# Performance work log

Hardware: AMD Instinct MI355X
Metric: run time of the kernel (lower is better)

The kernel has to match this reference:

```python
import jax, jax.numpy as jnp
import numpy as np

# static config (matches init_kwargs)
B, H, W = 8, 64, 64
DIM, NH = 512, 16
HD = DIM // NH
WS = 8            # square window
SHIFT = 4
N = WS * WS       # tokens per window
NW = (H // WS) * (W // WS)  # windows per image
SCALE = HD ** (-0.5)
MLP_HIDDEN = int(DIM * 4.0)


def _rel_pos_index():
    coords = np.stack(np.meshgrid(np.arange(WS), np.arange(WS), indexing='ij'))  # [2,Wh,Ww]
    cf = coords.reshape(2, -1)
    rel = cf[:, :, None] - cf[:, None, :]          # [2,N,N]
    rel = rel.transpose(1, 2, 0)                    # [N,N,2]
    rel[:, :, 0] += WS - 1
    rel[:, :, 1] += WS - 1
    rel[:, :, 0] *= 2 * WS - 1
    return rel.sum(-1)                              # [N,N]

REL_IDX = jnp.asarray(_rel_pos_index())


def _attn_mask():
    img_mask = np.zeros((1, H, W, 1), np.float32)
    slices = (slice(0, -WS), slice(-WS, -SHIFT), slice(-SHIFT, None))
    cnt = 0
    for hs in slices:
        for ws in slices:
            img_mask[:, hs, ws, :] = cnt
            cnt += 1
    m = img_mask.reshape(1, H // WS, WS, W // WS, WS, 1).transpose(0, 1, 3, 2, 4, 5).reshape(-1, N)
    am = m[:, None, :] - m[:, :, None]
    return jnp.asarray(np.where(am != 0, -100.0, 0.0).astype(np.float32))  # [NW,N,N]

ATTN_MASK = _attn_mask()


def layernorm(x, g, b, eps=1e-5):
    mu = x.mean(-1, keepdims=True)
    var = ((x - mu) ** 2).mean(-1, keepdims=True)
    return (x - mu) * jax.lax.rsqrt(var + eps) * g + b


def setup_inputs() -> dict:
    key = jax.random.key(0)
    ks = jax.random.split(key, 12)
    s = 0.02
    return {
        'x': jax.random.normal(ks[0], (B, H * W, DIM), jnp.float32),
        'fundamental_context': jax.random.normal(ks[1], (B, 64), jnp.float32),
        'norm1_g': jnp.ones((DIM,), jnp.float32),
        'norm1_b': jnp.zeros((DIM,), jnp.float32),
        'qkv_w': jax.random.normal(ks[2], (DIM, 3 * DIM), jnp.float32) * s,
        'qkv_b': jnp.zeros((3 * DIM,), jnp.float32),
        'rel_bias_table': jax.random.normal(ks[3], ((2 * WS - 1) ** 2, NH), jnp.float32) * s,
        'proj_w': jax.random.normal(ks[4], (DIM, DIM), jnp.float32) * s,
        'proj_b': jnp.zeros((DIM,), jnp.float32),
        'norm2_g': jnp.ones((DIM,), jnp.float32),
        'norm2_b': jnp.zeros((DIM,), jnp.float32),
        'fc1_w': jax.random.normal(ks[5], (DIM, MLP_HIDDEN), jnp.float32) * s,
        'fc1_b': jnp.zeros((MLP_HIDDEN,), jnp.float32),
        'fc2_w': jax.random.normal(ks[6], (MLP_HIDDEN, DIM), jnp.float32) * s,
        'fc2_b': jnp.zeros((DIM,), jnp.float32),
    }


def reference(x, fundamental_context, norm1_g, norm1_b, qkv_w, qkv_b,
              rel_bias_table, proj_w, proj_b, norm2_g, norm2_b,
              fc1_w, fc1_b, fc2_w, fc2_b):
    shortcut = x
    h = layernorm(x, norm1_g, norm1_b).reshape(B, H, W, DIM)
    # cyclic shift (SW-MSA)
    h = jnp.roll(h, (-SHIFT, -SHIFT), axis=(1, 2))
    # window partition -> [B*NW, N, C]
    win = h.reshape(B, H // WS, WS, W // WS, WS, DIM).transpose(0, 1, 3, 2, 4, 5)
    win = win.reshape(B * NW, N, DIM)
    # windowed multi-head attention
    qkv = (win @ qkv_w + qkv_b).reshape(B * NW, N, 3, NH, HD).transpose(2, 0, 3, 1, 4)
    q, k, v = qkv[0] * SCALE, qkv[1], qkv[2]          # [B_,NH,N,HD]
    attn = jnp.einsum('bhnd,bhmd->bhnm', q, k)        # [B_,NH,N,N]
    bias = rel_bias_table[REL_IDX.reshape(-1)].reshape(N, N, NH).transpose(2, 0, 1)
    attn = attn + bias[None]
    attn = attn.reshape(B, NW, NH, N, N) + ATTN_MASK[None, :, None]
    attn = jax.nn.softmax(attn.reshape(B * NW, NH, N, N), axis=-1)
    out = jnp.einsum('bhnm,bhmd->bhnd', attn, v).transpose(0, 2, 1, 3).reshape(B * NW, N, DIM)
    out = out @ proj_w + proj_b
    # window reverse -> [B,H,W,C]
    out = out.reshape(B, H // WS, W // WS, WS, WS, DIM).transpose(0, 1, 3, 2, 4, 5).reshape(B, H, W, DIM)
    # reverse cyclic shift
    out = jnp.roll(out, (SHIFT, SHIFT), axis=(1, 2)).reshape(B, H * W, DIM)
    x = shortcut + out
    # MLP block
    h = layernorm(x, norm2_g, norm2_b)
    h = jax.nn.gelu(h @ fc1_w + fc1_b, approximate=False) @ fc2_w + fc2_b
    return x + h
```

## Files before the change

### kernel.cpp

```cpp
#include <hip/hip_runtime.h>
#include <cstddef>
#include <cstdint>


typedef unsigned short u16;
typedef __attribute__((ext_vector_type(8))) short short8;
typedef __attribute__((ext_vector_type(4))) float floatx4;

__device__ __forceinline__ float bf2f(u16 u) {
    union { float f; unsigned i; } w; w.i = ((unsigned)u) << 16; return w.f;
}
__device__ __forceinline__ u16 f2bf(float f) {
    union { float f; unsigned i; } w; w.f = f;
    unsigned r = w.i + 0x7FFF + ((w.i >> 16) & 1);
    return (u16)(r >> 16);
}

__device__ __forceinline__ void gload_lds16(const u16* g, u16* l) {
    __builtin_amdgcn_global_load_lds(
        (const __attribute__((address_space(1))) void*)g,
        (__attribute__((address_space(3))) void*)l, 16, 0, 0);
}

__device__ __forceinline__ float erf_fast(float x) {
    float ax = fabsf(x);
    float t = 1.0f / (1.0f + 0.3275911f * ax);
    float poly = ((((1.061405429f * t - 1.453152027f) * t + 1.421413741f) * t
                   - 0.284496736f) * t + 0.254829592f) * t;
    float er = 1.0f - poly * __expf(-ax * ax);
    return copysignf(er, x);
}

__device__ __forceinline__ int win_to_img_row(int t) {
    int win = t >> 6, n = t & 63;
    int b = win >> 6, wr = (win >> 3) & 7, wc = win & 7;
    int h = ((wr << 3) + (n >> 3) + 4) & 63;
    int w = ((wc << 3) + (n & 7) + 4) & 63;
    return (b << 12) + (h << 6) + w;
}

__global__ __launch_bounds__(256) void ln_fused(
    const float* __restrict__ x, const float* __restrict__ g,
    const float* __restrict__ b, u16* __restrict__ out, int gather)
{
    int wave = threadIdx.x >> 6, lane = threadIdx.x & 63;
    int t = blockIdx.x * 4 + wave;
    int src = gather ? win_to_img_row(t) : t;
    const float* xr = x + (size_t)src * 512 + lane * 8;
    float4 a = *(const float4*)xr;
    float4 c = *(const float4*)(xr + 4);
    float s = a.x + a.y + a.z + a.w + c.x + c.y + c.z + c.w;
    float s2 = a.x*a.x + a.y*a.y + a.z*a.z + a.w*a.w
             + c.x*c.x + c.y*c.y + c.z*c.z + c.w*c.w;
#pragma unroll
    for (int off = 32; off; off >>= 1) { s += __shfl_down(s, off); s2 += __shfl_down(s2, off); }
    s = __shfl(s, 0); s2 = __shfl(s2, 0);
    float mu = s * (1.f / 512.f);
    float var = s2 * (1.f / 512.f) - mu * mu;
    float rs = rsqrtf(var + 1e-5f);
    int col = lane * 8;
    float4 g0 = *(const float4*)(g + col), g1 = *(const float4*)(g + col + 4);
    float4 b0 = *(const float4*)(b + col), b1 = *(const float4*)(b + col + 4);
    u16 r[8];
    r[0] = f2bf((a.x - mu) * rs * g0.x + b0.x);
    r[1] = f2bf((a.y - mu) * rs * g0.y + b0.y);
    r[2] = f2bf((a.z - mu) * rs * g0.z + b0.z);
    r[3] = f2bf((a.w - mu) * rs * g0.w + b0.w);
    r[4] = f2bf((c.x - mu) * rs * g1.x + b1.x);
    r[5] = f2bf((c.y - mu) * rs * g1.y + b1.y);
    r[6] = f2bf((c.z - mu) * rs * g1.z + b1.z);
    r[7] = f2bf((c.w - mu) * rs * g1.w + b1.w);
    *(uint4*)(out + (size_t)t * 512 + col) = *(const uint4*)r;
}

__global__ __launch_bounds__(256) void transpose_all(
    const float* __restrict__ qkv_w, const float* __restrict__ proj_w,
    const float* __restrict__ fc1_w, const float* __restrict__ fc2_w,
    u16* __restrict__ qkvT, u16* __restrict__ projT,
    u16* __restrict__ fc1T, u16* __restrict__ fc2T)
{
    int bid = blockIdx.x;
    const float* W; u16* WT; int K, N, base;
    if (bid < 384)       { W = qkv_w;  WT = qkvT;  K = 512;  N = 1536; base = 0; }
    else if (bid < 512)  { W = proj_w; WT = projT; K = 512;  N = 512;  base = 384; }
    else if (bid < 1024) { W = fc1_w;  WT = fc1T;  K = 512;  N = 2048; base = 512; }
    else                 { W = fc2_w;  WT = fc2T;  K = 2048; N = 512;  base = 1024; }
    int f = (bid - base) * 256 + threadIdx.x;
    int n = f % N, kc = f / N;
    if (kc >= (K >> 3)) return;
    int k0 = kc << 3;
    u16 r[8];
#pragma unroll
    for (int j = 0; j < 8; ++j) r[j] = f2bf(W[(size_t)(k0 + j) * N + n]);
    *(uint4*)(WT + (size_t)n * K + k0) = *(const uint4*)r;
}

enum { M_QKV = 0, M_PROJ = 1, M_GELU = 2, M_FINAL = 3 };

template <int MODE, int ASRC>
__global__ __launch_bounds__(256, 4) void gemm_bt(
    const u16* __restrict__ A, int lda,
    const u16* __restrict__ BT, int ldb,
    const float* __restrict__ bias,
    void* __restrict__ outp, const float* __restrict__ auxf, int K, int ldo)
{
    __shared__ __align__(16) u16 As[128 * 64];
    __shared__ __align__(16) u16 Bs[128 * 64];

    int tid = threadIdx.x;
    int nwg = gridDim.x * gridDim.y;
    int bid = blockIdx.y * gridDim.x + blockIdx.x;
    int q8 = nwg >> 3, r8 = nwg & 7;
    int xcd = bid & 7, pos = bid >> 3;
    int swz = (xcd < r8 ? xcd * (q8 + 1)
                        : r8 * (q8 + 1) + (xcd - r8) * q8) + pos;
    int bx = swz % gridDim.x, by = swz / gridDim.x;
    int bm = by * 128, bn = bx * 128;

    int wave = tid >> 6, lane = tid & 63;
    int quad = lane >> 4, lr = lane & 15;
    int wm = (wave >> 1) * 64, wn = (wave & 1) * 64;

    floatx4 acc[4][4] = {};

    for (int k0 = 0; k0 < K; k0 += 64) {
#pragma unroll
        for (int l = 0; l < 4; ++l) {
            int f = (l << 8) + tid;
            int row = f >> 3, c = f & 7;
            int cs = c ^ (row & 7);
            int kk = k0 + (cs << 3);
            const u16* gb = BT + (size_t)(bn + row) * ldb + kk;
            gload_lds16(gb, Bs + f * 8);
            if constexpr (ASRC == 0) {
                gload_lds16(A + (size_t)(bm + row) * lda + kk, As + f * 8);
            } else {
                int m = bm + row;
                gload_lds16(A + (size_t)(((m >> 6) << 4) + (kk >> 5)) * 2048
                              + (m & 63) * 32 + (kk & 31), As + f * 8);
            }
        }
        __syncthreads();
#pragma unroll
        for (int step = 0; step < 2; ++step) {
            short8 af[4], bv[4];
            int kc = step * 4 + quad;
#pragma unroll
            for (int t = 0; t < 4; ++t) {
                int ra = wm + t * 16 + lr;
                int rb = wn + t * 16 + lr;
                af[t] = *(const short8*)(As + ra * 64 + ((kc ^ (ra & 7)) << 3));
                bv[t] = *(const short8*)(Bs + rb * 64 + ((kc ^ (rb & 7)) << 3));
            }
#pragma unroll
            for (int mt = 0; mt < 4; ++mt)
#pragma unroll
                for (int nt = 0; nt < 4; ++nt)
                    acc[mt][nt] = __builtin_amdgcn_mfma_f32_16x16x32_bf16(
                        af[mt], bv[nt], acc[mt][nt], 0, 0, 0);
        }
        __syncthreads();
    }

#pragma unroll
    for (int mt = 0; mt < 4; ++mt) {
#pragma unroll
        for (int nt = 0; nt < 4; ++nt) {
            int m0 = bm + wm + mt * 16 + quad * 4;
            int n = bn + wn + nt * 16 + lr;
#pragma unroll
            for (int i = 0; i < 4; ++i) {
                int m = m0 + i;
                float v = acc[mt][nt][i];
                if constexpr (MODE == M_QKV) {
                    v += bias[n];
                    int sel = n >> 9, head = (n >> 5) & 15, d = n & 31;
                    int wh = (m >> 6) * 16 + head, tok = m & 63;
                    ((u16*)outp)[(size_t)sel * 16777216 + (size_t)wh * 2048 + tok * 32 + d] = f2bf(v);
                } else if constexpr (MODE == M_PROJ) {
                    size_t idx = (size_t)win_to_img_row(m) * 512 + n;
                    ((float*)outp)[idx] = v + bias[n] + auxf[idx];
                } else if constexpr (MODE == M_GELU) {
                    v += bias[n];
                    float gel = 0.5f * v * (1.0f + erf_fast(v * 0.70710678118654752f));
                    ((u16*)outp)[(size_t)m * ldo + n] = f2bf(gel);
                } else {
                    size_t idx = (size_t)m * 512 + n;
                    float* o = (float*)outp;
                    float bb = bias ? bias[n] : 0.0f;
                    o[idx] = o[idx] + v + bb;
                }
            }
        }
    }
}

__global__ __launch_bounds__(256) void attn_mfma(
    const u16* __restrict__ qkv, const float* __restrict__ table,
    u16* __restrict__ outp)
{
    __shared__ __align__(8) u16 PT[4][64 * 76];
    __shared__ float blds[225];

    int w = threadIdx.x >> 6, lane = threadIdx.x & 63;
    int head = blockIdx.x & 15, win = ((blockIdx.x >> 4) << 2) + w;
    int wh = (win << 4) + head;
    int quad = lane >> 4, lr = lane & 15;
    const u16* qb = qkv + (size_t)wh * 2048;
    const u16* kb = qb + 16777216;
    const u16* vb = qb + 33554432;
    u16* PTw = PT[w];

    for (int i = threadIdx.x; i < 225; i += 256) blds[i] = table[i * 16 + head];
    __syncthreads();

    short8 qf[4], kf[4];
#pragma unroll
    for (int t = 0; t < 4; ++t) {
        qf[t] = *(const short8*)(qb + (t * 16 + lr) * 32 + quad * 8);
        kf[t] = *(const short8*)(kb + (t * 16 + lr) * 32 + quad * 8);
    }
    floatx4 s[4][4] = {};
#pragma unroll
    for (int mi = 0; mi < 4; ++mi)
#pragma unroll
        for (int ni = 0; ni < 4; ++ni)
            s[mi][ni] = __builtin_amdgcn_mfma_f32_16x16x32_bf16(qf[mi], kf[ni], s[mi][ni], 0, 0, 0);

    short8 vf[2][2];
#pragma unroll
    for (int ks = 0; ks < 2; ++ks)
#pragma unroll
        for (int nd = 0; nd < 2; ++nd)
#pragma unroll
            for (int j = 0; j < 8; ++j)
                vf[ks][nd][j] = (short)vb[(ks * 32 + quad * 8 + j) * 32 + nd * 16 + lr];

    int wr = (win >> 3) & 7, wc = win & 7;
    int rj[4], cj[4], regj[4];
#pragma unroll
    for (int ni = 0; ni < 4; ++ni) {
        int kj = ni * 16 + lr;
        rj[ni] = kj >> 3; cj[ni] = kj & 7;
        int hJ = wr * 8 + rj[ni], wJ = wc * 8 + cj[ni];
        regj[ni] = (hJ < 56 ? 0 : (hJ < 60 ? 1 : 2)) * 3 + (wJ < 56 ? 0 : (wJ < 60 ? 1 : 2));
    }
    float rm[4][4], linv[4][4];
#pragma unroll
    for (int mi = 0; mi < 4; ++mi) {
#pragma unroll
        for (int i = 0; i < 4; ++i) {
            int qi = mi * 16 + quad * 4 + i;
            int ri = qi >> 3, ci = qi & 7;
            int hI = wr * 8 + ri, wI = wc * 8 + ci;
            int regi = (hI < 56 ? 0 : (hI < 60 ? 1 : 2)) * 3 + (wI < 56 ? 0 : (wI < 60 ? 1 : 2));
            float mx = -1e30f;
#pragma unroll
            for (int ni = 0; ni < 4; ++ni) {
                float v = s[mi][ni][i] * 0.17677669529663687f
                        + blds[(ri - rj[ni] + 7) * 15 + (ci - cj[ni] + 7)];
                if (regj[ni] != regi) v -= 100.f;
                s[mi][ni][i] = v;
                mx = fmaxf(mx, v);
            }
            rm[mi][i] = mx;
        }
    }
#pragma unroll
    for (int mi = 0; mi < 4; ++mi)
#pragma unroll
        for (int i = 0; i < 4; ++i) {
            float mx = rm[mi][i];
#pragma unroll
            for (int msk = 1; msk < 16; msk <<= 1) mx = fmaxf(mx, __shfl_xor(mx, msk));
            float sum = 0.f;
#pragma unroll
            for (int ni = 0; ni < 4; ++ni) {
                float e = __expf(s[mi][ni][i] - mx);
                s[mi][ni][i] = e;
                sum += e;
            }
#pragma unroll
            for (int msk = 1; msk < 16; msk <<= 1) sum += __shfl_xor(sum, msk);
            linv[mi][i] = 1.f / sum;
        }

#pragma unroll
    for (int mi = 0; mi < 4; ++mi)
#pragma unroll
        for (int ni = 0; ni < 4; ++ni) {
            unsigned lo = (unsigned)f2bf(s[mi][ni][0]) | ((unsigned)f2bf(s[mi][ni][1]) << 16);
            unsigned hi = (unsigned)f2bf(s[mi][ni][2]) | ((unsigned)f2bf(s[mi][ni][3]) << 16);
            uint2 pk = make_uint2(lo, hi);
            *(uint2*)(PTw + (ni * 16 + lr) * 76 + mi * 16 + quad * 4) = pk;
        }
    __syncthreads();

    floatx4 o[4][2] = {};
#pragma unroll
    for (int mi = 0; mi < 4; ++mi) {
#pragma unroll
        for (int ks = 0; ks < 2; ++ks) {
            short8 pa;
#pragma unroll
            for (int j = 0; j < 8; ++j)
                pa[j] = (short)PTw[(ks * 32 + quad * 8 + j) * 76 + mi * 16 + lr];
#pragma unroll
            for (int nd = 0; nd < 2; ++nd)
                o[mi][nd] = __builtin_amdgcn_mfma_f32_16x16x32_bf16(pa, vf[ks][nd], o[mi][nd], 0, 0, 0);
        }
    }
    u16* ob = outp + (size_t)wh * 2048;
#pragma unroll
    for (int mi = 0; mi < 4; ++mi)
#pragma unroll
        for (int nd = 0; nd < 2; ++nd)
#pragma unroll
            for (int i = 0; i < 4; ++i) {
                int qi = mi * 16 + quad * 4 + i;
                ob[qi * 32 + nd * 16 + lr] = f2bf(o[mi][nd][i] * linv[mi][i]);
            }
}

extern "C" void kernel_launch(void* const* d_in, const int* in_sizes, int n_in,
                              void* d_out, int out_size, void* d_ws, size_t ws_size,
                              hipStream_t stream)
{
    (void)in_sizes; (void)n_in; (void)out_size; (void)ws_size;
    const float* x      = (const float*)d_in[0];
    const float* n1g    = (const float*)d_in[2];
    const float* n1b    = (const float*)d_in[3];
    const float* qkv_w  = (const float*)d_in[4];
    const float* qkv_b  = (const float*)d_in[5];
    const float* table  = (const float*)d_in[6];
    const float* proj_w = (const float*)d_in[7];
    const float* proj_b = (const float*)d_in[8];
    const float* n2g    = (const float*)d_in[9];
    const float* n2b    = (const float*)d_in[10];
    const float* fc1_w  = (const float*)d_in[11];
    const float* fc1_b  = (const float*)d_in[12];
    const float* fc2_w  = (const float*)d_in[13];
    const float* fc2_b  = (const float*)d_in[14];
    float* out = (float*)d_out;
    char* ws = (char*)d_ws;

    u16* qkvT  = (u16*)ws;
    u16* projT = qkvT + 786432;
    u16* fc1T  = projT + 262144;
    u16* fc2T  = fc1T + 1048576;
    u16* q    = (u16*)(ws + 8388608);
    u16* h2   = q;
    u16* gbuf = q + 16777216;
    u16* xw   = (u16*)d_out;

    transpose_all<<<1536, 256, 0, stream>>>(
        qkv_w, proj_w, fc1_w, fc2_w, qkvT, projT, fc1T, fc2T);

    ln_fused<<<8192, 256, 0, stream>>>(x, n1g, n1b, xw, 1);
    gemm_bt<M_QKV, 0><<<dim3(12, 256), 256, 0, stream>>>(
        xw, 512, qkvT, 512, qkv_b, q, nullptr, 512, 0);
    attn_mfma<<<2048, 256, 0, stream>>>(q, table, q);
    gemm_bt<M_PROJ, 3><<<dim3(4, 256), 256, 0, stream>>>(
        q, 0, projT, 512, proj_b, out, x, 512, 0);
    ln_fused<<<8192, 256, 0, stream>>>(out, n2g, n2b, h2, 0);
    for (int nc = 0; nc < 2; ++nc) {
        gemm_bt<M_GELU, 0><<<dim3(8, 256), 256, 0, stream>>>(
            h2, 512, fc1T + (size_t)nc * 1024 * 512, 512,
            fc1_b + nc * 1024, gbuf, nullptr, 512, 1024);
        gemm_bt<M_FINAL, 0><<<dim3(4, 256), 256, 0, stream>>>(
            gbuf, 1024, fc2T + nc * 1024, 2048,
            (nc == 0 ? fc2_b : nullptr), out, nullptr, 1024, 0);
    }
}
```

Measured before the change: 510.1 us.

## Split MLP over M instead of hidden dim, add 64-row tile for fc2

The MLP now processes two halves of the token rows, each with the full 2048-wide hidden layer, instead of splitting the hidden dimension into two chunks. This removes the read-modify-write accumulation of the fc2 output across chunks and the null-bias branch. The GEMM kernel gains a template M tile size, and fc2 uses 64-row tiles so its grid stays large enough to fill the GPU. The cost is a larger gbuf footprint per chunk and smaller per-wave MFMA reuse in the fc2 GEMM.

```diff
diff --git a/kernel.cpp b/kernel.cpp
--- a/kernel.cpp
+++ b/kernel.cpp
@@ -97,14 +97,15 @@
 
 enum { M_QKV = 0, M_PROJ = 1, M_GELU = 2, M_FINAL = 3 };
 
-template <int MODE, int ASRC>
+template <int MODE, int ASRC, int MT = 128>
 __global__ __launch_bounds__(256, 4) void gemm_bt(
     const u16* __restrict__ A, int lda,
     const u16* __restrict__ BT, int ldb,
     const float* __restrict__ bias,
     void* __restrict__ outp, const float* __restrict__ auxf, int K, int ldo)
 {
-    __shared__ __align__(16) u16 As[128 * 64];
+    constexpr int MSUB = MT / 32;
+    __shared__ __align__(16) u16 As[MT * 64];
     __shared__ __align__(16) u16 Bs[128 * 64];
 
     int tid = threadIdx.x;
@@ -115,23 +116,27 @@
     int swz = (xcd < r8 ? xcd * (q8 + 1)
                         : r8 * (q8 + 1) + (xcd - r8) * q8) + pos;
     int bx = swz % gridDim.x, by = swz / gridDim.x;
-    int bm = by * 128, bn = bx * 128;
+    int bm = by * MT, bn = bx * 128;
 
     int wave = tid >> 6, lane = tid & 63;
     int quad = lane >> 4, lr = lane & 15;
-    int wm = (wave >> 1) * 64, wn = (wave & 1) * 64;
-
-    floatx4 acc[4][4] = {};
+    int wm = (wave >> 1) * (MT / 2), wn = (wave & 1) * 64;
+
+    floatx4 acc[MSUB][4] = {};
 
     for (int k0 = 0; k0 < K; k0 += 64) {
 #pragma unroll
         for (int l = 0; l < 4; ++l) {
             int f = (l << 8) + tid;
             int row = f >> 3, c = f & 7;
-            int cs = c ^ (row & 7);
-            int kk = k0 + (cs << 3);
-            const u16* gb = BT + (size_t)(bn + row) * ldb + kk;
-            gload_lds16(gb, Bs + f * 8);
+            int kk = k0 + ((c ^ (row & 7)) << 3);
+            gload_lds16(BT + (size_t)(bn + row) * ldb + kk, Bs + f * 8);
+        }
+#pragma unroll
+        for (int l = 0; l < MT / 32; ++l) {
+            int f = (l << 8) + tid;
+            int row = f >> 3, c = f & 7;
+            int kk = k0 + ((c ^ (row & 7)) << 3);
             if constexpr (ASRC == 0) {
                 gload_lds16(A + (size_t)(bm + row) * lda + kk, As + f * 8);
             } else {
@@ -143,17 +148,20 @@
         __syncthreads();
 #pragma unroll
         for (int step = 0; step < 2; ++step) {
-            short8 af[4], bv[4];
+            short8 af[MSUB], bv[4];
             int kc = step * 4 + quad;
 #pragma unroll
+            for (int t = 0; t < MSUB; ++t) {
+                int ra = wm + t * 16 + lr;
+                af[t] = *(const short8*)(As + ra * 64 + ((kc ^ (ra & 7)) << 3));
+            }
+#pragma unroll
             for (int t = 0; t < 4; ++t) {
-                int ra = wm + t * 16 + lr;
                 int rb = wn + t * 16 + lr;
-                af[t] = *(const short8*)(As + ra * 64 + ((kc ^ (ra & 7)) << 3));
                 bv[t] = *(const short8*)(Bs + rb * 64 + ((kc ^ (rb & 7)) << 3));
             }
 #pragma unroll
-            for (int mt = 0; mt < 4; ++mt)
+            for (int mt = 0; mt < MSUB; ++mt)
 #pragma unroll
                 for (int nt = 0; nt < 4; ++nt)
                     acc[mt][nt] = __builtin_amdgcn_mfma_f32_16x16x32_bf16(
@@ -163,7 +171,7 @@
     }
 
 #pragma unroll
-    for (int mt = 0; mt < 4; ++mt) {
+    for (int mt = 0; mt < MSUB; ++mt) {
 #pragma unroll
         for (int nt = 0; nt < 4; ++nt) {
             int m0 = bm + wm + mt * 16 + quad * 4;
@@ -187,8 +195,7 @@
                 } else {
                     size_t idx = (size_t)m * 512 + n;
                     float* o = (float*)outp;
-                    float bb = bias ? bias[n] : 0.0f;
-                    o[idx] = o[idx] + v + bb;
+                    o[idx] = o[idx] + v + bias[n];
                 }
             }
         }
@@ -363,12 +370,12 @@
     gemm_bt<M_PROJ, 3><<<dim3(4, 256), 256, 0, stream>>>(
         q, 0, projT, 512, proj_b, out, x, 512, 0);
     ln_fused<<<8192, 256, 0, stream>>>(out, n2g, n2b, h2, 0);
-    for (int nc = 0; nc < 2; ++nc) {
-        gemm_bt<M_GELU, 0><<<dim3(8, 256), 256, 0, stream>>>(
-            h2, 512, fc1T + (size_t)nc * 1024 * 512, 512,
-            fc1_b + nc * 1024, gbuf, nullptr, 512, 1024);
-        gemm_bt<M_FINAL, 0><<<dim3(4, 256), 256, 0, stream>>>(
-            gbuf, 1024, fc2T + nc * 1024, 2048,
-            (nc == 0 ? fc2_b : nullptr), out, nullptr, 1024, 0);
-    }
-}
+    for (int mc = 0; mc < 2; ++mc) {
+        gemm_bt<M_GELU, 0><<<dim3(16, 128), 256, 0, stream>>>(
+            h2 + (size_t)mc * 16384 * 512, 512, fc1T, 512, fc1_b,
+            gbuf, nullptr, 512, 2048);
+        gemm_bt<M_FINAL, 0, 64><<<dim3(4, 256), 256, 0, stream>>>(
+            gbuf, 2048, fc2T, 2048, fc2_b,
+            out + (size_t)mc * 16384 * 512, nullptr, 2048, 0);
+    }
+}
```

Measured after the change: 498.9 us. 1.02x faster.
